# Kernel optimization log

Measured on AMD Instinct MI355X. Metric: run time of the kernel, lower is better.

Reference implementation:

```python
import jax, jax.numpy as jnp
import numpy as np

DIM = 768
N_HEADS = 12
HEAD_DIM = DIM // N_HEADS
SCALE = HEAD_DIM ** -0.5


def setup_inputs() -> dict:
    key = jax.random.key(0)
    ks = jax.random.split(key, 5)
    B, N = 8, 1024
    x = jax.random.normal(ks[0], (B, N, DIM), dtype=jnp.float32)
    # Linear weights stored as (in, out) for x @ W; torch stores (out, in).
    w_qkv = jax.random.normal(ks[1], (DIM, 3 * DIM), dtype=jnp.float32) * (DIM ** -0.5)
    b_qkv = jnp.zeros((3 * DIM,), dtype=jnp.float32)
    w_proj = jax.random.normal(ks[2], (DIM, DIM), dtype=jnp.float32) * (DIM ** -0.5)
    b_proj = jnp.zeros((DIM,), dtype=jnp.float32)
    return {"x": x, "w_qkv": w_qkv, "b_qkv": b_qkv, "w_proj": w_proj, "b_proj": b_proj}


def reference(x, w_qkv, b_qkv, w_proj, b_proj):
    B, N, _ = x.shape
    qkv = x @ w_qkv + b_qkv                       # [B, N, 3*dim]
    qkv = qkv.reshape(B, N, 3, N_HEADS, HEAD_DIM)
    qkv = jnp.transpose(qkv, (2, 0, 3, 1, 4))     # [3, B, H, N, hd]
    q, k, v = qkv[0], qkv[1], qkv[2]
    attn = jnp.einsum("bhqd,bhkd->bhqk", q, k) * SCALE
    attn = jax.nn.softmax(attn, axis=-1)
    out = jnp.einsum("bhqk,bhkd->bhqd", attn, v)  # [B, H, N, hd]
    out = jnp.transpose(out, (0, 2, 1, 3)).reshape(B, N, DIM)
    return out @ w_proj + b_proj
```

## Files before the change

kernel.cpp:

```cpp
#include <hip/hip_runtime.h>
#include <cstdint>

#define DIM 768
#define NH 12
#define HD 64
#define SEQ 1024
#define NBH 96

#define QOFF  ((size_t)0)
#define KOFF  ((size_t)6291456)
#define VOFF  ((size_t)12582912)
#define AOFF  ((size_t)18874368)
#define XOFF  ((size_t)25165824)
#define WQOFF ((size_t)31457280)
#define WPOFF ((size_t)33226752)

#define QSCALE 0.18033688f

#define WAIT_VM0   __builtin_amdgcn_s_waitcnt(0x0F70)
#define WAIT_VM(n) __builtin_amdgcn_s_waitcnt(0x0F70 | (n))
#define BAR        __builtin_amdgcn_s_barrier()
#define CFENCE     __asm__ __volatile__("" ::: "memory")

typedef __attribute__((ext_vector_type(8))) __bf16 bf16x8;
typedef __attribute__((ext_vector_type(2))) __bf16 bf16x2;
typedef __attribute__((ext_vector_type(4))) float f32x4;
typedef __attribute__((ext_vector_type(4))) short s16x4;
typedef unsigned short u16;

__device__ __forceinline__ u16 f2bf(float f) {
    union { float f; unsigned u; } x; x.f = f;
    unsigned r = x.u + 0x7fffu + ((x.u >> 16) & 1u);
    return (u16)(r >> 16);
}

__device__ __forceinline__ unsigned pkbf(float a, float b) {
#if __has_builtin(__builtin_amdgcn_cvt_pk_bf16_f32)
    bf16x2 v = __builtin_amdgcn_cvt_pk_bf16_f32(a, b);
    union { bf16x2 v; unsigned u; } c; c.v = v; return c.u;
#else
    return (unsigned)f2bf(a) | ((unsigned)f2bf(b) << 16);
#endif
}

__device__ __forceinline__ void async_cp16(const void* g, void* l) {
    __builtin_amdgcn_global_load_lds((const __attribute__((address_space(1))) void*)g,
                                     (__attribute__((address_space(3))) void*)l, 16, 0, 0);
}

__global__ __launch_bounds__(256) void prep(const float* __restrict__ x,
                                            const float* __restrict__ wq,
                                            const float* __restrict__ wp,
                                            u16* __restrict__ ws) {
    const int bid = blockIdx.x;
    const int tid = threadIdx.x;
    if (bid < 3072) {
        size_t i = (size_t)bid * 512 + tid;
#pragma unroll
        for (int j = 0; j < 2; ++j, i += 256) {
            float4 v = *(const float4*)&x[i * 4];
            ushort4 o;
            o.x = f2bf(v.x); o.y = f2bf(v.y); o.z = f2bf(v.z); o.w = f2bf(v.w);
            *(ushort4*)&ws[XOFF + i * 4] = o;
        }
        return;
    }
    __shared__ float T[64][65];
    const float* w; u16* wt; int N, bx, by;
    if (bid < 3504) { int b = bid - 3072; w = wq; wt = ws + WQOFF; N = 2304; bx = b % 36; by = b / 36; }
    else            { int b = bid - 3504; w = wp; wt = ws + WPOFF; N = 768;  bx = b % 12; by = b / 12; }
    const int K = 768;
    const int k0 = by * 64, n0 = bx * 64;
    const int r = tid >> 4, c4 = (tid & 15) * 4;
#pragma unroll
    for (int i = 0; i < 4; ++i) {
        float4 v = *(const float4*)&w[(size_t)(k0 + r + 16 * i) * N + n0 + c4];
        T[r + 16 * i][c4 + 0] = v.x; T[r + 16 * i][c4 + 1] = v.y;
        T[r + 16 * i][c4 + 2] = v.z; T[r + 16 * i][c4 + 3] = v.w;
    }
    __syncthreads();
#pragma unroll
    for (int i = 0; i < 4; ++i) {
        int rr = r + 16 * i;
        ushort4 o;
        o.x = f2bf(T[c4 + 0][rr]); o.y = f2bf(T[c4 + 1][rr]);
        o.z = f2bf(T[c4 + 2][rr]); o.w = f2bf(T[c4 + 3][rr]);
        *(ushort4*)&wt[(size_t)(n0 + rr) * K + k0 + c4] = o;
    }
}

template <int EPI>
__global__ __launch_bounds__(512, 2) void gemm_bt(const u16* __restrict__ A,
                                                  const u16* __restrict__ Bt,
                                                  const float* __restrict__ bias,
                                                  float* __restrict__ outf,
                                                  u16* __restrict__ outq) {
    constexpr int NT = 12;
    __shared__ __align__(16) u16 As[4][128 * 64];
    __shared__ __align__(16) u16 Bs[4][128 * 64];
    const int tid = threadIdx.x;
    const int lane = tid & 63;
    const int w = tid >> 6;
    const int wm = w >> 2, wn = w & 3;

    const int gx = gridDim.x;
    const int flat = blockIdx.y * gx + blockIdx.x;
    const int chunk = (gx * gridDim.y) >> 3;
    const int nf = (flat & 7) * chunk + (flat >> 3);
    const int bxs = nf % gx, bys = nf / gx;
    const int m0 = bys * 128, n0 = bxs * 128;

    const int lgrp = lane >> 3;
    const int gg = (lane & 7) ^ lgrp;
    const u16* ga = A  + (size_t)(m0 + w * 16 + lgrp) * 768 + gg * 8;
    const u16* gb = Bt + (size_t)(n0 + w * 16 + lgrp) * 768 + gg * 8;

    const int l15 = lane & 15, qg = lane >> 4, q4 = qg * 4;

    int aoff[4][2], boff[2][2];
#pragma unroll
    for (int r = 0; r < 4; ++r) {
        int row = 64 * wm + 16 * r + l15;
#pragma unroll
        for (int kc = 0; kc < 2; ++kc)
            aoff[r][kc] = row * 64 + (((4 * kc + qg) ^ (row & 7)) << 3);
    }
#pragma unroll
    for (int c = 0; c < 2; ++c) {
        int row = 32 * wn + 16 * c + l15;
#pragma unroll
        for (int kc = 0; kc < 2; ++kc)
            boff[c][kc] = row * 64 + (((4 * kc + qg) ^ (row & 7)) << 3);
    }

    f32x4 acc[4][2] = {};

    auto stageT = [&](int t) {
        const int buf = t & 3;
        const size_t ko = (size_t)t * 64;
#pragma unroll
        for (int i = 0; i < 2; ++i) {
            async_cp16(ga + (size_t)i * 8 * 768 + ko, &As[buf][(w * 16 + i * 8) * 64]);
            async_cp16(gb + (size_t)i * 8 * 768 + ko, &Bs[buf][(w * 16 + i * 8) * 64]);
        }
    };
    auto compute = [&](int buf) {
#pragma unroll
        for (int kc = 0; kc < 2; ++kc) {
            bf16x8 af[4], bfr[2];
#pragma unroll
            for (int r = 0; r < 4; ++r) af[r] = *(const bf16x8*)&As[buf][aoff[r][kc]];
#pragma unroll
            for (int c = 0; c < 2; ++c) bfr[c] = *(const bf16x8*)&Bs[buf][boff[c][kc]];
            __builtin_amdgcn_s_setprio(1);
#pragma unroll
            for (int r = 0; r < 4; ++r)
#pragma unroll
                for (int c = 0; c < 2; ++c)
                    acc[r][c] = __builtin_amdgcn_mfma_f32_16x16x32_bf16(af[r], bfr[c], acc[r][c], 0, 0, 0);
            __builtin_amdgcn_s_setprio(0);
        }
    };

    stageT(0); stageT(1); stageT(2);

    int t = 0;
    for (; t < NT - 3; ++t) {
        WAIT_VM(8);
        BAR;
        CFENCE;
        stageT(t + 3);
        compute(t & 3);
    }
    WAIT_VM(8); BAR; CFENCE; compute(t & 3); ++t;
    WAIT_VM(4); BAR; CFENCE; compute(t & 3); ++t;
    WAIT_VM0;   BAR; CFENCE; compute(t & 3);

#pragma unroll
    for (int r = 0; r < 4; ++r) {
#pragma unroll
        for (int c = 0; c < 2; ++c) {
            const int cg = n0 + 32 * wn + 16 * c + l15;
            const float bv = bias[cg];
            const int mb = m0 + 64 * wm + 16 * r + q4;
            if constexpr (EPI == 0) {
#pragma unroll
                for (int g = 0; g < 4; ++g)
                    outf[(size_t)(mb + g) * DIM + cg] = acc[r][c][g] + bv;
            } else {
                const int which = (cg >= 1536) ? 2 : (cg >= 768 ? 1 : 0);
                const int rem = cg - which * 768;
                const int h = rem >> 6, d = rem & 63;
                const int b = mb >> 10, q = mb & 1023;
                if (which == 0) {
#pragma unroll
                    for (int g = 0; g < 4; ++g)
                        outq[QOFF + ((size_t)(b * NH + h) * SEQ + q + g) * HD + d] =
                            f2bf((acc[r][c][g] + bv) * QSCALE);
                } else if (which == 1) {
#pragma unroll
                    for (int g = 0; g < 4; ++g)
                        outq[KOFF + ((size_t)(b * NH + h) * SEQ + q + g) * HD + d] =
                            f2bf(acc[r][c][g] + bv);
                } else {
                    ushort4 pk;
                    pk.x = f2bf(acc[r][c][0] + bv); pk.y = f2bf(acc[r][c][1] + bv);
                    pk.z = f2bf(acc[r][c][2] + bv); pk.w = f2bf(acc[r][c][3] + bv);
                    *(ushort4*)&outq[VOFF + ((size_t)(b * NH + h) * HD + d) * SEQ + q] = pk;
                }
            }
        }
    }
}

__global__ __launch_bounds__(256) void flash_attn(const u16* __restrict__ ws, u16* __restrict__ attn_out) {
    __shared__ __align__(16) u16 Ks[2][64 * 64];
    __shared__ __align__(16) u16 Vs[2][64 * 64];

    const int tid = threadIdx.x;
    const int lane = tid & 63;
    const int wv = tid >> 6;
    const int qt = blockIdx.x;
    const int bh = blockIdx.y;
    const u16* qp = ws + QOFF + (size_t)bh * SEQ * HD;
    const u16* kp = ws + KOFF + (size_t)bh * SEQ * HD;
    const u16* vp = ws + VOFF + (size_t)bh * HD * SEQ;

    const int l15 = lane & 15, qg = lane >> 4, q8 = qg * 8;
    const int l7 = l15 & 7;

    bf16x8 bq[2][2];
#pragma unroll
    for (int r = 0; r < 2; ++r)
#pragma unroll
        for (int kc = 0; kc < 2; ++kc)
            bq[r][kc] = *(const bf16x8*)&qp[(size_t)(qt * 128 + 32 * wv + 16 * r + l15) * HD + 32 * kc + q8];

    const int lgrp = lane >> 3;
    const int gg = (lane & 7) ^ lgrp;
    auto stage = [&](int buf, int ktv) {
#pragma unroll
        for (int i = 0; i < 2; ++i) {
            async_cp16(kp + (size_t)(ktv * 64 + wv * 16 + i * 8 + lgrp) * 64 + gg * 8,
                       &Ks[buf][(wv * 16 + i * 8) * 64]);
            async_cp16(vp + (size_t)(wv * 16 + i * 8 + lgrp) * SEQ + ktv * 64 + gg * 8,
                       &Vs[buf][(wv * 16 + i * 8) * 64]);
        }
    };
    stage(0, 0);

    int akoff[4][2], avoff[4][4];
#pragma unroll
    for (int c = 0; c < 4; ++c) {
#pragma unroll
        for (int kc = 0; kc < 2; ++kc)
            akoff[c][kc] = (16 * c + l15) * 64 + (((4 * kc + qg) ^ l7) << 3);
#pragma unroll
        for (int cd = 0; cd < 4; ++cd)
            avoff[c][cd] = (16 * cd + l15) * 64 + (((2 * c + (qg >> 1)) ^ l7) << 3) + (qg & 1) * 4;
    }

    f32x4 oacc[2][4] = {};
    float lsum[2] = {0.f, 0.f};

    for (int kt = 0; kt < 16; ++kt) {
        const int cur = kt & 1;
        WAIT_VM0;
        BAR;
        CFENCE;
        if (kt < 15) stage(cur ^ 1, kt + 1);

        f32x4 sacc[4][2] = {};
#pragma unroll
        for (int c = 0; c < 4; ++c) {
#pragma unroll
            for (int kc = 0; kc < 2; ++kc) {
                bf16x8 ak = *(const bf16x8*)&Ks[cur][akoff[c][kc]];
#pragma unroll
                for (int r = 0; r < 2; ++r)
                    sacc[c][r] = __builtin_amdgcn_mfma_f32_16x16x32_bf16(ak, bq[r][kc], sacc[c][r], 0, 0, 0);
            }
        }

        s16x4 pf[4][2];
#pragma unroll
        for (int c = 0; c < 4; ++c) {
#pragma unroll
            for (int r = 0; r < 2; ++r) {
                float p0 = __builtin_amdgcn_exp2f(sacc[c][r][0]);
                float p1 = __builtin_amdgcn_exp2f(sacc[c][r][1]);
                float p2 = __builtin_amdgcn_exp2f(sacc[c][r][2]);
                float p3 = __builtin_amdgcn_exp2f(sacc[c][r][3]);
                lsum[r] += (p0 + p1) + (p2 + p3);
                union { uint2 u; s16x4 v; } pk;
                pk.u.x = pkbf(p0, p1); pk.u.y = pkbf(p2, p3);
                pf[c][r] = pk.v;
            }
        }

#pragma unroll
        for (int c = 0; c < 4; ++c) {
            s16x4 av[4];
#pragma unroll
            for (int cd = 0; cd < 4; ++cd)
                av[cd] = *(const s16x4*)&Vs[cur][avoff[c][cd]];
#pragma unroll
            for (int r = 0; r < 2; ++r)
#pragma unroll
                for (int cd = 0; cd < 4; ++cd)
                    oacc[r][cd] = __builtin_amdgcn_mfma_f32_16x16x16bf16_1k(av[cd], pf[c][r], oacc[r][cd], 0, 0, 0);
        }
    }

#pragma unroll
    for (int r = 0; r < 2; ++r) {
        lsum[r] += __shfl_xor(lsum[r], 16);
        lsum[r] += __shfl_xor(lsum[r], 32);
    }

    const int b = bh / NH, h = bh % NH;
#pragma unroll
    for (int r = 0; r < 2; ++r) {
        const float inv = 1.f / lsum[r];
        const int qrow = qt * 128 + 32 * wv + 16 * r + l15;
        u16* orow = attn_out + (size_t)(b * SEQ + qrow) * DIM + h * HD + qg * 4;
#pragma unroll
        for (int cd = 0; cd < 4; ++cd) {
            ushort4 o;
            o.x = f2bf(oacc[r][cd][0] * inv); o.y = f2bf(oacc[r][cd][1] * inv);
            o.z = f2bf(oacc[r][cd][2] * inv); o.w = f2bf(oacc[r][cd][3] * inv);
            *(ushort4*)&orow[16 * cd] = o;
        }
    }
}

extern "C" void kernel_launch(void* const* d_in, const int* in_sizes, int n_in,
                              void* d_out, int out_size, void* d_ws, size_t ws_size,
                              hipStream_t stream) {
    const float* x      = (const float*)d_in[0];
    const float* w_qkv  = (const float*)d_in[1];
    const float* b_qkv  = (const float*)d_in[2];
    const float* w_proj = (const float*)d_in[3];
    const float* b_proj = (const float*)d_in[4];
    float* out = (float*)d_out;
    u16* ws = (u16*)d_ws;

    prep<<<3648, 256, 0, stream>>>(x, w_qkv, w_proj, ws);
    gemm_bt<1><<<dim3(18, 64), 512, 0, stream>>>(ws + XOFF, ws + WQOFF, b_qkv, nullptr, ws);
    flash_attn<<<dim3(8, 96), 256, 0, stream>>>(ws, ws + AOFF);
    gemm_bt<0><<<dim3(6, 64), 512, 0, stream>>>(ws + AOFF, ws + WPOFF, b_proj, out, nullptr);
}
```

Baseline: 209.6 us.

## Split K/V waits in attention and use smaller-tile GEMM for output projection

The flash attention stage now issues the K loads before the V loads and waits only on the K copies before the QK^T step. It then waits on the V copies with a second barrier just before the PV step, so the V transfer can overlap the score and exp computation. The output projection moves to a new 256-thread GEMM with 128x64 tiles and a 12x64 grid. That gives more blocks than the previous 6x64 launch on the 512-thread kernel, to improve CU occupancy for this small-N GEMM. The new GEMM is single-buffered and syncs twice per K step, and the extra barrier in attention adds some cost per iteration.

```diff
diff --git a/kernel.cpp b/kernel.cpp
--- a/kernel.cpp
+++ b/kernel.cpp
@@ -90,7 +90,7 @@
 }
 
 template <int EPI>
-__global__ __launch_bounds__(512, 2) void gemm_bt(const u16* __restrict__ A,
+__global__ __launch_bounds__(512, 2) void gemm512(const u16* __restrict__ A,
                                                   const u16* __restrict__ Bt,
                                                   const float* __restrict__ bias,
                                                   float* __restrict__ outf,
@@ -213,6 +213,108 @@
     }
 }
 
+template <int EPI, int NC>
+__global__ __launch_bounds__(256, 3) void gemm256(const u16* __restrict__ A,
+                                                  const u16* __restrict__ Bt,
+                                                  const float* __restrict__ bias,
+                                                  float* __restrict__ outf,
+                                                  u16* __restrict__ outq) {
+    __shared__ __align__(16) u16 As[128 * 64];
+    __shared__ __align__(16) u16 Bs[32 * NC * 64];
+    const int tid = threadIdx.x;
+    const int lane = tid & 63;
+    const int w = tid >> 6;
+    const int wm = w >> 1, wn = w & 1;
+    const int m0 = blockIdx.y * 128, n0 = blockIdx.x * (32 * NC);
+
+    const int lgrp = lane >> 3;
+    const int gg = (lane & 7) ^ lgrp;
+    const u16* ga = A  + (size_t)(m0 + w * 32 + lgrp) * 768 + gg * 8;
+    const u16* gb = Bt + (size_t)(n0 + w * 8 * NC + lgrp) * 768 + gg * 8;
+    u16* lba = As + w * 32 * 64;
+    u16* lbb = Bs + w * 8 * NC * 64;
+
+    const int l15 = lane & 15, qg = lane >> 4, q4 = qg * 4;
+
+    int aoff[4][2], boff[NC][2];
+#pragma unroll
+    for (int r = 0; r < 4; ++r) {
+        int row = 64 * wm + 16 * r + l15;
+#pragma unroll
+        for (int kc = 0; kc < 2; ++kc)
+            aoff[r][kc] = row * 64 + (((4 * kc + qg) ^ (row & 7)) << 3);
+    }
+#pragma unroll
+    for (int c = 0; c < NC; ++c) {
+        int row = 16 * NC * wn + 16 * c + l15;
+#pragma unroll
+        for (int kc = 0; kc < 2; ++kc)
+            boff[c][kc] = row * 64 + (((4 * kc + qg) ^ (row & 7)) << 3);
+    }
+
+    f32x4 acc[4][NC] = {};
+
+    for (int k0 = 0; k0 < 768; k0 += 64) {
+#pragma unroll
+        for (int i = 0; i < 4; ++i)
+            async_cp16(ga + (size_t)i * 8 * 768 + k0, lba + i * 512);
+#pragma unroll
+        for (int i = 0; i < NC; ++i)
+            async_cp16(gb + (size_t)i * 8 * 768 + k0, lbb + i * 512);
+        __syncthreads();
+#pragma unroll
+        for (int kc = 0; kc < 2; ++kc) {
+            bf16x8 af[4], bfr[NC];
+#pragma unroll
+            for (int r = 0; r < 4; ++r) af[r] = *(const bf16x8*)&As[aoff[r][kc]];
+#pragma unroll
+            for (int c = 0; c < NC; ++c) bfr[c] = *(const bf16x8*)&Bs[boff[c][kc]];
+#pragma unroll
+            for (int r = 0; r < 4; ++r)
+#pragma unroll
+                for (int c = 0; c < NC; ++c)
+                    acc[r][c] = __builtin_amdgcn_mfma_f32_16x16x32_bf16(af[r], bfr[c], acc[r][c], 0, 0, 0);
+        }
+        __syncthreads();
+    }
+
+#pragma unroll
+    for (int r = 0; r < 4; ++r) {
+#pragma unroll
+        for (int c = 0; c < NC; ++c) {
+            const int cg = n0 + 16 * NC * wn + 16 * c + l15;
+            const float bv = bias[cg];
+            const int mb = m0 + 64 * wm + 16 * r + q4;
+            if constexpr (EPI == 0) {
+#pragma unroll
+                for (int g = 0; g < 4; ++g)
+                    outf[(size_t)(mb + g) * DIM + cg] = acc[r][c][g] + bv;
+            } else {
+                const int which = (cg >= 1536) ? 2 : (cg >= 768 ? 1 : 0);
+                const int rem = cg - which * 768;
+                const int h = rem >> 6, d = rem & 63;
+                const int b = mb >> 10, q = mb & 1023;
+                if (which == 0) {
+#pragma unroll
+                    for (int g = 0; g < 4; ++g)
+                        outq[QOFF + ((size_t)(b * NH + h) * SEQ + q + g) * HD + d] =
+                            f2bf((acc[r][c][g] + bv) * QSCALE);
+                } else if (which == 1) {
+#pragma unroll
+                    for (int g = 0; g < 4; ++g)
+                        outq[KOFF + ((size_t)(b * NH + h) * SEQ + q + g) * HD + d] =
+                            f2bf(acc[r][c][g] + bv);
+                } else {
+                    ushort4 pk;
+                    pk.x = f2bf(acc[r][c][0] + bv); pk.y = f2bf(acc[r][c][1] + bv);
+                    pk.z = f2bf(acc[r][c][2] + bv); pk.w = f2bf(acc[r][c][3] + bv);
+                    *(ushort4*)&outq[VOFF + ((size_t)(b * NH + h) * HD + d) * SEQ + q] = pk;
+                }
+            }
+        }
+    }
+}
+
 __global__ __launch_bounds__(256) void flash_attn(const u16* __restrict__ ws, u16* __restrict__ attn_out) {
     __shared__ __align__(16) u16 Ks[2][64 * 64];
     __shared__ __align__(16) u16 Vs[2][64 * 64];
@@ -240,12 +342,13 @@
     const int gg = (lane & 7) ^ lgrp;
     auto stage = [&](int buf, int ktv) {
 #pragma unroll
-        for (int i = 0; i < 2; ++i) {
+        for (int i = 0; i < 2; ++i)
             async_cp16(kp + (size_t)(ktv * 64 + wv * 16 + i * 8 + lgrp) * 64 + gg * 8,
                        &Ks[buf][(wv * 16 + i * 8) * 64]);
+#pragma unroll
+        for (int i = 0; i < 2; ++i)
             async_cp16(vp + (size_t)(wv * 16 + i * 8 + lgrp) * SEQ + ktv * 64 + gg * 8,
                        &Vs[buf][(wv * 16 + i * 8) * 64]);
-        }
     };
     stage(0, 0);
 
@@ -265,7 +368,7 @@
 
     for (int kt = 0; kt < 16; ++kt) {
         const int cur = kt & 1;
-        WAIT_VM0;
+        WAIT_VM(2);
         BAR;
         CFENCE;
         if (kt < 15) stage(cur ^ 1, kt + 1);
@@ -298,6 +401,11 @@
             }
         }
 
+        if (kt < 15) { WAIT_VM(4); }
+        else         { WAIT_VM0;   }
+        BAR;
+        CFENCE;
+
 #pragma unroll
         for (int c = 0; c < 4; ++c) {
             s16x4 av[4];
@@ -346,7 +454,7 @@
     u16* ws = (u16*)d_ws;
 
     prep<<<3648, 256, 0, stream>>>(x, w_qkv, w_proj, ws);
-    gemm_bt<1><<<dim3(18, 64), 512, 0, stream>>>(ws + XOFF, ws + WQOFF, b_qkv, nullptr, ws);
+    gemm512<1><<<dim3(18, 64), 512, 0, stream>>>(ws + XOFF, ws + WQOFF, b_qkv, nullptr, ws);
     flash_attn<<<dim3(8, 96), 256, 0, stream>>>(ws, ws + AOFF);
-    gemm_bt<0><<<dim3(6, 64), 512, 0, stream>>>(ws + AOFF, ws + WPOFF, b_proj, out, nullptr);
-}
+    gemm256<0, 2><<<dim3(12, 64), 256, 0, stream>>>(ws + AOFF, ws + WPOFF, b_proj, out, nullptr);
+}
```

After: 209.1 us. No clear change (-0.3%).
